# Kernel optimization log

Hardware: AMD Instinct MI355X
Metric: run time of the kernel (lower is better)

## Reference

```python
import jax, jax.numpy as jnp
import numpy as np

B, C, L = 8, 512, 8192
H = 8  # head_count
DK = C // H  # head key channels
DV = C // H  # head value channels


def setup_inputs() -> dict:
    key = jax.random.key(0)
    ks = jax.random.split(key, 10)
    s = 1.0 / np.sqrt(C)
    return {
        "input_": jax.random.normal(ks[0], (B, C, L), jnp.float32),
        "context_": jax.random.normal(ks[1], (B, C, L), jnp.float32),
        "Wk": jax.random.normal(ks[2], (C, C), jnp.float32) * s,
        "bk": jax.random.normal(ks[3], (C,), jnp.float32) * 0.01,
        "Wq": jax.random.normal(ks[4], (C, C), jnp.float32) * s,
        "bq": jax.random.normal(ks[5], (C,), jnp.float32) * 0.01,
        "Wv": jax.random.normal(ks[6], (C, C), jnp.float32) * s,
        "bv": jax.random.normal(ks[7], (C,), jnp.float32) * 0.01,
        "Wr": jax.random.normal(ks[8], (C, C), jnp.float32) * s,
        "br": jax.random.normal(ks[9], (C,), jnp.float32) * 0.01,
    }


def _proj(W, b, x):
    # 1x1 Conv1d == channel matmul: [O,C] x [B,C,L] -> [B,O,L]
    return jnp.einsum('oc,bcl->bol', W, x) + b[None, :, None]


def reference(input_, context_, Wk, bk, Wq, bq, Wv, bv, Wr, br):
    b, _, l = input_.shape
    keys = _proj(Wk, bk, context_).reshape(b, H, DK, l)
    queries = _proj(Wq, bq, input_).reshape(b, H, DK, l)
    values = _proj(Wv, bv, context_).reshape(b, H, DV, l)
    # per-head: softmax(K) over sequence, softmax(Q) over head-key channels
    k = jax.nn.softmax(keys, axis=3)
    q = jax.nn.softmax(queries, axis=2)
    # context = K @ V^T : [b,h,dk,dv]
    ctx = jnp.einsum('bhkl,bhvl->bhkv', k, values)
    # attended = context^T @ Q : [b,h,dv,l]
    att = jnp.einsum('bhkv,bhkl->bhvl', ctx, q).reshape(b, H * DV, l)
    return _proj(Wr, br, att) + input_
```

## Files before the change

kernel.cpp:

```cpp
#include <hip/hip_runtime.h>

#define NB 8
#define NC 512
#define NL 8192
#define NH 8
#define ND 64

typedef float f32x4 __attribute__((ext_vector_type(4)));
typedef __bf16 bf16x8 __attribute__((ext_vector_type(8)));
typedef unsigned int u32x4 __attribute__((ext_vector_type(4)));

__device__ __forceinline__ unsigned short f2bf(float f) {
    unsigned u = __builtin_bit_cast(unsigned, f);
    u += 0x7fffu + ((u >> 16) & 1u);
    return (unsigned short)(u >> 16);
}
__device__ __forceinline__ float bf2f_lo(unsigned w) {
    return __builtin_bit_cast(float, w << 16);
}
__device__ __forceinline__ float bf2f_hi(unsigned w) {
    return __builtin_bit_cast(float, w & 0xffff0000u);
}
__device__ __forceinline__ bf16x8 frag_from_u32x4(u32x4 v) {
    return __builtin_bit_cast(bf16x8, v);
}
__device__ __forceinline__ bf16x8 ld_frag_lds(const unsigned short* p) {
    const unsigned* q = (const unsigned*)p;
    u32x4 v = { q[0], q[1], q[2], q[3] };
    return frag_from_u32x4(v);
}
__device__ __forceinline__ bf16x8 ld_frag_g16(const unsigned short* p) {
    return frag_from_u32x4(*(const u32x4*)p);
}

__device__ __forceinline__ void gload16(const unsigned short* g, unsigned short* l) {
    __builtin_amdgcn_global_load_lds(
        (const __attribute__((address_space(1))) unsigned int*)g,
        (__attribute__((address_space(3))) unsigned int*)l, 16, 0, 0);
}

__global__ __launch_bounds__(256) void cvt_w_kernel(const float* __restrict__ s,
                                                    unsigned short* __restrict__ d, int n) {
    int i = blockIdx.x * 256 + threadIdx.x;
    if (i < n) d[i] = f2bf(s[i]);
}

__global__ __launch_bounds__(256) void zero_kernel(float* __restrict__ p, int n) {
    int i = blockIdx.x * 256 + threadIdx.x;
    if (i < n) p[i] = 0.f;
}

__global__ __launch_bounds__(256) void concat_bias_kernel(const float* __restrict__ a,
                                                          const float* __restrict__ b,
                                                          float* __restrict__ d) {
    int i = blockIdx.x * 256 + threadIdx.x;
    d[i] = (i < NC) ? a[i] : b[i - NC];
}

__device__ __forceinline__ int ltidx(int c, int l) {
    return c * 64 + ((((l) >> 2) ^ ((c >> 2) & 15)) << 2) + (l & 3);
}
__global__ __launch_bounds__(256) void transpose_cvt_kernel(
    const float* __restrict__ X, unsigned short* __restrict__ Y)
{
    const int b = blockIdx.z;
    const int l0 = blockIdx.x * 64, c0 = blockIdx.y * 64;
    const int t = threadIdx.x;
    __shared__ alignas(16) unsigned short lt[64 * 64];
    const float* Xb = X + (size_t)b * NC * NL;
    #pragma unroll
    for (int it = 0; it < 4; ++it) {
        const int c = it * 16 + (t >> 4), l4 = (t & 15) * 4;
        f32x4 v = *(const f32x4*)(Xb + (size_t)(c0 + c) * NL + l0 + l4);
        unsigned lo = f2bf(v.x) | ((unsigned)f2bf(v.y) << 16);
        unsigned hi = f2bf(v.z) | ((unsigned)f2bf(v.w) << 16);
        unsigned* p = (unsigned*)&lt[ltidx(c, l4)];
        p[0] = lo; p[1] = hi;
    }
    __syncthreads();
    unsigned short* Yb = Y + (size_t)b * NL * NC;
    #pragma unroll
    for (int it = 0; it < 2; ++it) {
        const int l = it * 32 + (t >> 3), c8 = (t & 7) * 8;
        u32x4 o;
        #pragma unroll
        for (int d = 0; d < 4; ++d) {
            unsigned lo = lt[ltidx(c8 + 2 * d, l)];
            unsigned hi = lt[ltidx(c8 + 2 * d + 1, l)];
            o[d] = lo | (hi << 16);
        }
        *(u32x4*)(Yb + (size_t)(l0 + l) * NC + c0 + c8) = o;
    }
}

template<int MT, bool RESID, bool PERB, bool QSMT>
__global__ __launch_bounds__(256) void gemm_kernel(
    const unsigned short* __restrict__ Wb,
    const unsigned short* __restrict__ Xt,
    const float* __restrict__ bias,
    const float* __restrict__ resid,
    void* __restrict__ Yv)
{
    const int bx = blockIdx.x;
    const int g  = bx >> 3;
    const int mt = g % MT;
    const int nt = (g / MT) * 8 + (bx & 7);
    const int b  = blockIdx.y;
    const int t  = threadIdx.x;
    const int wave = t >> 6, lane = t & 63;
    const int m0 = mt * 128, n0 = nt * 128;
    const int wm = (wave & 1) * 64, wn = (wave >> 1) * 64;
    const int OC = MT * 128;

    __shared__ alignas(16) unsigned short lA[128 * 32];
    __shared__ alignas(16) unsigned short lX[128 * 32];

    f32x4 acc[4][4] = {};

    const unsigned short* Wp = Wb + (PERB ? (size_t)b * NC * NC : 0);
    const unsigned short* Xb = Xt + (size_t)b * NL * NC;

    const int lr = lane & 15, q = lane >> 4;
    const unsigned aoff = (unsigned)((wm + lr) * 64 + (q ^ (((wm + lr) >> 1) & 3)) * 16);
    const unsigned boff = (unsigned)((wn + lr) * 64 + (q ^ (((wn + lr) >> 1) & 3)) * 16);
    const int pb0 = wave * 128;

    for (int k0 = 0; k0 < NC; k0 += 32) {
        #pragma unroll
        for (int cc = 0; cc < 2; ++cc) {
            const int pb = pb0 + cc * 64;
            const int p  = pb + lane;
            const int r  = p >> 2;
            const int qq = (p & 3) ^ ((r >> 1) & 3);
            gload16(Wp + (size_t)(m0 + r) * NC + k0 + qq * 8, &lA[pb * 8]);
            gload16(Xb + (size_t)(n0 + r) * NC + k0 + qq * 8, &lX[pb * 8]);
        }
        __syncthreads();

        bf16x8 af[4], bfx[4];
        #pragma unroll
        for (int i = 0; i < 4; ++i)
            af[i] = frag_from_u32x4(*(const u32x4*)((const char*)lA + aoff + i * 1024));
        #pragma unroll
        for (int j = 0; j < 4; ++j)
            bfx[j] = frag_from_u32x4(*(const u32x4*)((const char*)lX + boff + j * 1024));
        #pragma unroll
        for (int i = 0; i < 4; ++i)
            #pragma unroll
            for (int j = 0; j < 4; ++j)
                acc[i][j] = __builtin_amdgcn_mfma_f32_16x16x32_bf16(af[i], bfx[j], acc[i][j], 0, 0, 0);
        __syncthreads();
    }

    const int col = lane & 15, row0 = (lane >> 4) * 4;

    if constexpr (QSMT) {
        #pragma unroll
        for (int i = 0; i < 4; ++i)
            #pragma unroll
            for (int r = 0; r < 4; ++r) {
                const float bo = bias[m0 + wm + i * 16 + row0 + r];
                #pragma unroll
                for (int j = 0; j < 4; ++j) acc[i][j][r] += bo;
            }
        float inv[4];
        #pragma unroll
        for (int j = 0; j < 4; ++j) {
            float m = -1e30f;
            #pragma unroll
            for (int i = 0; i < 4; ++i)
                #pragma unroll
                for (int r = 0; r < 4; ++r) m = fmaxf(m, acc[i][j][r]);
            m = fmaxf(m, __shfl_xor(m, 16));
            m = fmaxf(m, __shfl_xor(m, 32));
            float s = 0.f;
            #pragma unroll
            for (int i = 0; i < 4; ++i)
                #pragma unroll
                for (int r = 0; r < 4; ++r) {
                    const float e = __expf(acc[i][j][r] - m);
                    acc[i][j][r] = e;
                    s += e;
                }
            s += __shfl_xor(s, 16);
            s += __shfl_xor(s, 32);
            inv[j] = 1.0f / s;
        }
        unsigned short* Yq = (unsigned short*)Yv;
        #pragma unroll
        for (int j = 0; j < 4; ++j) {
            const size_t rowb = (size_t)b * NL * NC + (size_t)(n0 + wn + j * 16 + col) * NC;
            #pragma unroll
            for (int i = 0; i < 4; ++i) {
                const int o0 = m0 + wm + i * 16 + row0;
                unsigned lo = f2bf(acc[i][j][0] * inv[j]) | ((unsigned)f2bf(acc[i][j][1] * inv[j]) << 16);
                unsigned hi = f2bf(acc[i][j][2] * inv[j]) | ((unsigned)f2bf(acc[i][j][3] * inv[j]) << 16);
                *(unsigned long long*)(Yq + rowb + o0) =
                    (unsigned long long)lo | ((unsigned long long)hi << 32);
            }
        }
    } else {
        #pragma unroll
        for (int i = 0; i < 4; ++i) {
            #pragma unroll
            for (int r = 0; r < 4; ++r) {
                const int o = m0 + wm + i * 16 + row0 + r;
                const float bo = bias[o];
                const size_t rb = (size_t)b * OC * NL + (size_t)o * NL + n0 + wn;
                if constexpr (RESID) {
                    float* Y = (float*)Yv;
                    #pragma unroll
                    for (int j = 0; j < 4; ++j) {
                        const size_t idx = rb + j * 16 + col;
                        Y[idx] = acc[i][j][r] + bo + resid[idx];
                    }
                } else {
                    unsigned short* Y = (unsigned short*)Yv;
                    #pragma unroll
                    for (int j = 0; j < 4; ++j)
                        Y[rb + j * 16 + col] = f2bf(acc[i][j][r] + bo);
                }
            }
        }
    }
}

__global__ __launch_bounds__(256) void softmax_rows(unsigned short* __restrict__ KV) {
    const int row = blockIdx.x;
    const int t = threadIdx.x;
    const int wave = t >> 6, lane = t & 63;
    unsigned short* p = KV + ((size_t)(row >> 9) * 2 * NC + (row & 511)) * NL;

    float v[32];
    float mx = -1e30f;
    #pragma unroll
    for (int i = 0; i < 4; ++i) {
        u32x4 raw = *(const u32x4*)(p + (size_t)(i * 256 + t) * 8);
        #pragma unroll
        for (int d = 0; d < 4; ++d) {
            unsigned w = raw[d];
            v[i * 8 + d * 2]     = bf2f_lo(w);
            v[i * 8 + d * 2 + 1] = bf2f_hi(w);
        }
        #pragma unroll
        for (int j = 0; j < 8; ++j) mx = fmaxf(mx, v[i * 8 + j]);
    }
    #pragma unroll
    for (int off = 32; off > 0; off >>= 1) mx = fmaxf(mx, __shfl_down(mx, off));
    __shared__ float red[16];
    if (lane == 0) red[wave] = mx;
    __syncthreads();
    mx = fmaxf(fmaxf(red[0], red[1]), fmaxf(red[2], red[3]));

    float s = 0.f;
    #pragma unroll
    for (int i = 0; i < 32; ++i) { v[i] = __expf(v[i] - mx); s += v[i]; }
    #pragma unroll
    for (int off = 32; off > 0; off >>= 1) s += __shfl_down(s, off);
    if (lane == 0) red[8 + wave] = s;
    __syncthreads();
    s = red[8] + red[9] + red[10] + red[11];
    const float inv = 1.0f / s;

    #pragma unroll
    for (int i = 0; i < 4; ++i) {
        u32x4 outw;
        #pragma unroll
        for (int d = 0; d < 4; ++d) {
            unsigned lo = f2bf(v[i * 8 + d * 2] * inv);
            unsigned hi = f2bf(v[i * 8 + d * 2 + 1] * inv);
            outw[d] = lo | (hi << 16);
        }
        *(u32x4*)(p + (size_t)(i * 256 + t) * 8) = outw;
    }
}

__global__ __launch_bounds__(256) void ctx_kernel(
    const unsigned short* __restrict__ KV,
    float* __restrict__ ctx)
{
    const int bh = blockIdx.x;
    const int sp = blockIdx.y;
    const int t = threadIdx.x;
    const int wave = t >> 6, lane = t & 63;
    const int b = bh >> 3, h = bh & 7;
    const size_t base_k = ((size_t)b * 2 * NC + h * ND) * NL;
    const size_t base_v = base_k + (size_t)NC * NL;
    const int i = wave * 16 + (lane & 15);
    const int koff = (lane >> 4) * 8;
    const unsigned short* Ka = KV + base_k + (size_t)i * NL + koff;

    f32x4 acc[4] = {};
    const int l0 = sp * (NL / 16);
    for (int l = l0; l < l0 + (NL / 16); l += 32) {
        bf16x8 a = ld_frag_g16(Ka + l);
        #pragma unroll
        for (int j = 0; j < 4; ++j) {
            bf16x8 bv = ld_frag_g16(KV + base_v + (size_t)(j * 16 + (lane & 15)) * NL + l + koff);
            acc[j] = __builtin_amdgcn_mfma_f32_16x16x32_bf16(a, bv, acc[j], 0, 0, 0);
        }
    }
    const int col = lane & 15, row0 = (lane >> 4) * 4;
    #pragma unroll
    for (int j = 0; j < 4; ++j)
        #pragma unroll
        for (int r = 0; r < 4; ++r)
            atomicAdd(&ctx[(size_t)bh * (ND * ND) + (size_t)(wave * 16 + row0 + r) * ND + j * 16 + col],
                      acc[j][r]);
}

__global__ __launch_bounds__(512) void fold_kernel(
    const unsigned short* __restrict__ Wrb,
    const float* __restrict__ ctxb,
    unsigned short* __restrict__ Mb)
{
    const int bh = blockIdx.x;
    const int b = bh >> 3, h = bh & 7;
    const int t = threadIdx.x;
    const int wave = t >> 6, lane = t & 63;

    __shared__ unsigned short lc[64 * 66];
    const float* cs = ctxb + (size_t)bh * (ND * ND);
    #pragma unroll
    for (int it = 0; it < 8; ++it) {
        int i = it * 512 + t;
        lc[(i >> 6) * 66 + (i & 63)] = f2bf(cs[i]);
    }
    __syncthreads();

    const int koff = (lane >> 4) * 8;
    f32x4 acc[4][4] = {};
    #pragma unroll
    for (int kk = 0; kk < 64; kk += 32) {
        bf16x8 af[4], bfx[4];
        #pragma unroll
        for (int i = 0; i < 4; ++i)
            af[i] = ld_frag_g16(Wrb + (size_t)(wave * 64 + i * 16 + (lane & 15)) * NC
                                + h * ND + kk + koff);
        #pragma unroll
        for (int j = 0; j < 4; ++j)
            bfx[j] = ld_frag_lds(&lc[(j * 16 + (lane & 15)) * 66 + kk + koff]);
        #pragma unroll
        for (int i = 0; i < 4; ++i)
            #pragma unroll
            for (int j = 0; j < 4; ++j)
                acc[i][j] = __builtin_amdgcn_mfma_f32_16x16x32_bf16(af[i], bfx[j], acc[i][j], 0, 0, 0);
    }

    const int col = lane & 15, row0 = (lane >> 4) * 4;
    #pragma unroll
    for (int i = 0; i < 4; ++i)
        #pragma unroll
        for (int r = 0; r < 4; ++r) {
            const int o = wave * 64 + i * 16 + row0 + r;
            #pragma unroll
            for (int j = 0; j < 4; ++j)
                Mb[(size_t)b * NC * NC + (size_t)o * NC + h * ND + j * 16 + col]
                    = f2bf(acc[i][j][r]);
        }
}

extern "C" void kernel_launch(void* const* d_in, const int* in_sizes, int n_in,
                              void* d_out, int out_size, void* d_ws, size_t ws_size,
                              hipStream_t stream) {
    (void)in_sizes; (void)n_in; (void)out_size; (void)ws_size;
    const float* input_   = (const float*)d_in[0];
    const float* context_ = (const float*)d_in[1];
    const float* Wk = (const float*)d_in[2];
    const float* bk = (const float*)d_in[3];
    const float* Wq = (const float*)d_in[4];
    const float* bq = (const float*)d_in[5];
    const float* Wv = (const float*)d_in[6];
    const float* bv = (const float*)d_in[7];
    const float* Wr = (const float*)d_in[8];
    const float* br = (const float*)d_in[9];
    float* out = (float*)d_out;

    char* ws = (char*)d_ws;
    unsigned short* Wkvb = (unsigned short*)ws;
    unsigned short* Wqb  = Wkvb + 2 * NC * NC;
    unsigned short* Wrb  = Wqb + NC * NC;
    float* bkv  = (float*)(Wrb + NC * NC);
    float* ctxb = bkv + 2 * NC;
    unsigned short* KVp = (unsigned short*)(ctxb + NB * NH * ND * ND);
    unsigned short* R2  = KVp + (size_t)NB * 2 * NC * NL;
    unsigned short* Mb  = KVp;
    unsigned short* Xt_in = (unsigned short*)d_out;

    const int wN = NC * NC;
    cvt_w_kernel<<<wN / 256, 256, 0, stream>>>(Wk, Wkvb, wN);
    cvt_w_kernel<<<wN / 256, 256, 0, stream>>>(Wv, Wkvb + wN, wN);
    cvt_w_kernel<<<wN / 256, 256, 0, stream>>>(Wq, Wqb, wN);
    cvt_w_kernel<<<wN / 256, 256, 0, stream>>>(Wr, Wrb, wN);
    concat_bias_kernel<<<4, 256, 0, stream>>>(bk, bv, bkv);
    zero_kernel<<<(NB * NH * ND * ND) / 256, 256, 0, stream>>>(ctxb, NB * NH * ND * ND);

    transpose_cvt_kernel<<<dim3(NL / 64, NC / 64, NB), 256, 0, stream>>>(context_, R2);

    gemm_kernel<8, false, false, false><<<dim3(64 * 8, NB), 256, 0, stream>>>(
        Wkvb, R2, bkv, nullptr, KVp);

    transpose_cvt_kernel<<<dim3(NL / 64, NC / 64, NB), 256, 0, stream>>>(input_, Xt_in);

    gemm_kernel<4, false, false, true><<<dim3(64 * 4, NB), 256, 0, stream>>>(
        Wqb, Xt_in, bq, nullptr, R2);

    softmax_rows<<<NB * NC, 256, 0, stream>>>(KVp);
    ctx_kernel<<<dim3(NB * NH, 16), 256, 0, stream>>>(KVp, ctxb);
    fold_kernel<<<NB * NH, 512, 0, stream>>>(Wrb, ctxb, Mb);

    gemm_kernel<4, true, true, false><<<dim3(64 * 4, NB), 256, 0, stream>>>(
        Mb, R2, br, input_, out);
}
```

Before: 654.6 us.

## Fuse key softmax into KV GEMM epilogue, merge prep and transpose launches, widen K tile

```diff
diff --git a/kernel.cpp b/kernel.cpp
--- a/kernel.cpp
+++ b/kernel.cpp
@@ -15,12 +15,6 @@
     u += 0x7fffu + ((u >> 16) & 1u);
     return (unsigned short)(u >> 16);
 }
-__device__ __forceinline__ float bf2f_lo(unsigned w) {
-    return __builtin_bit_cast(float, w << 16);
-}
-__device__ __forceinline__ float bf2f_hi(unsigned w) {
-    return __builtin_bit_cast(float, w & 0xffff0000u);
-}
 __device__ __forceinline__ bf16x8 frag_from_u32x4(u32x4 v) {
     return __builtin_bit_cast(bf16x8, v);
 }
@@ -39,31 +33,38 @@
         (__attribute__((address_space(3))) unsigned int*)l, 16, 0, 0);
 }
 
-__global__ __launch_bounds__(256) void cvt_w_kernel(const float* __restrict__ s,
-                                                    unsigned short* __restrict__ d, int n) {
+__global__ __launch_bounds__(256) void prep_kernel(
+    const float* __restrict__ Wk, const float* __restrict__ Wv,
+    const float* __restrict__ Wq, const float* __restrict__ Wr,
+    const float* __restrict__ bk, const float* __restrict__ bv,
+    unsigned short* __restrict__ Wb,
+    float* __restrict__ bkv,
+    float* __restrict__ zf)
+{
+    const int WN = NC * NC;
     int i = blockIdx.x * 256 + threadIdx.x;
-    if (i < n) d[i] = f2bf(s[i]);
-}
-
-__global__ __launch_bounds__(256) void zero_kernel(float* __restrict__ p, int n) {
-    int i = blockIdx.x * 256 + threadIdx.x;
-    if (i < n) p[i] = 0.f;
-}
-
-__global__ __launch_bounds__(256) void concat_bias_kernel(const float* __restrict__ a,
-                                                          const float* __restrict__ b,
-                                                          float* __restrict__ d) {
-    int i = blockIdx.x * 256 + threadIdx.x;
-    d[i] = (i < NC) ? a[i] : b[i - NC];
+    if (i < 4 * WN) {
+        const float* src = (i < WN) ? Wk : (i < 2 * WN) ? Wv : (i < 3 * WN) ? Wq : Wr;
+        Wb[i] = f2bf(src[i & (WN - 1)]);
+    } else if (i < 4 * WN + 2 * NC) {
+        int j = i - 4 * WN;
+        bkv[j] = (j < NC) ? bk[j] : bv[j - NC];
+    } else {
+        zf[i - (4 * WN + 2 * NC)] = 0.f;
+    }
 }
 
 __device__ __forceinline__ int ltidx(int c, int l) {
     return c * 64 + ((((l) >> 2) ^ ((c >> 2) & 15)) << 2) + (l & 3);
 }
 __global__ __launch_bounds__(256) void transpose_cvt_kernel(
-    const float* __restrict__ X, unsigned short* __restrict__ Y)
+    const float* __restrict__ X0, const float* __restrict__ X1,
+    unsigned short* __restrict__ Y0, unsigned short* __restrict__ Y1)
 {
-    const int b = blockIdx.z;
+    const int bz = blockIdx.z;
+    const float* X = (bz < NB) ? X0 : X1;
+    unsigned short* Y = (bz < NB) ? Y0 : Y1;
+    const int b = bz & (NB - 1);
     const int l0 = blockIdx.x * 64, c0 = blockIdx.y * 64;
     const int t = threadIdx.x;
     __shared__ alignas(16) unsigned short lt[64 * 64];
@@ -93,13 +94,14 @@
     }
 }
 
-template<int MT, bool RESID, bool PERB, bool QSMT>
+template<int MT, bool RESID, bool PERB, bool QSMT, bool EXPK>
 __global__ __launch_bounds__(256) void gemm_kernel(
     const unsigned short* __restrict__ Wb,
     const unsigned short* __restrict__ Xt,
     const float* __restrict__ bias,
     const float* __restrict__ resid,
-    void* __restrict__ Yv)
+    void* __restrict__ Yv,
+    float* __restrict__ rowsum)
 {
     const int bx = blockIdx.x;
     const int g  = bx >> 3;
@@ -112,8 +114,8 @@
     const int wm = (wave & 1) * 64, wn = (wave >> 1) * 64;
     const int OC = MT * 128;
 
-    __shared__ alignas(16) unsigned short lA[128 * 32];
-    __shared__ alignas(16) unsigned short lX[128 * 32];
+    __shared__ alignas(16) unsigned short lA[128 * 64];
+    __shared__ alignas(16) unsigned short lX[128 * 64];
 
     f32x4 acc[4][4] = {};
 
@@ -121,34 +123,38 @@
     const unsigned short* Xb = Xt + (size_t)b * NL * NC;
 
     const int lr = lane & 15, q = lane >> 4;
-    const unsigned aoff = (unsigned)((wm + lr) * 64 + (q ^ (((wm + lr) >> 1) & 3)) * 16);
-    const unsigned boff = (unsigned)((wn + lr) * 64 + (q ^ (((wn + lr) >> 1) & 3)) * 16);
-    const int pb0 = wave * 128;
-
-    for (int k0 = 0; k0 < NC; k0 += 32) {
-        #pragma unroll
-        for (int cc = 0; cc < 2; ++cc) {
-            const int pb = pb0 + cc * 64;
+    const unsigned abase = (unsigned)((wm + lr) * 128);
+    const unsigned bbase = (unsigned)((wn + lr) * 128);
+    const unsigned sw = (unsigned)(lr & 7);
+
+    for (int k0 = 0; k0 < NC; k0 += 64) {
+        #pragma unroll
+        for (int cc = 0; cc < 4; ++cc) {
+            const int pb = wave * 256 + cc * 64;
             const int p  = pb + lane;
-            const int r  = p >> 2;
-            const int qq = (p & 3) ^ ((r >> 1) & 3);
+            const int r  = p >> 3;
+            const int qq = (p & 7) ^ (r & 7);
             gload16(Wp + (size_t)(m0 + r) * NC + k0 + qq * 8, &lA[pb * 8]);
             gload16(Xb + (size_t)(n0 + r) * NC + k0 + qq * 8, &lX[pb * 8]);
         }
         __syncthreads();
 
-        bf16x8 af[4], bfx[4];
-        #pragma unroll
-        for (int i = 0; i < 4; ++i)
-            af[i] = frag_from_u32x4(*(const u32x4*)((const char*)lA + aoff + i * 1024));
-        #pragma unroll
-        for (int j = 0; j < 4; ++j)
-            bfx[j] = frag_from_u32x4(*(const u32x4*)((const char*)lX + boff + j * 1024));
-        #pragma unroll
-        for (int i = 0; i < 4; ++i)
+        #pragma unroll
+        for (int kk = 0; kk < 2; ++kk) {
+            const unsigned cq = (((unsigned)(kk * 4 + q)) ^ sw) * 16;
+            bf16x8 af[4], bfx[4];
+            #pragma unroll
+            for (int i = 0; i < 4; ++i)
+                af[i] = frag_from_u32x4(*(const u32x4*)((const char*)lA + abase + i * 2048 + cq));
             #pragma unroll
             for (int j = 0; j < 4; ++j)
-                acc[i][j] = __builtin_amdgcn_mfma_f32_16x16x32_bf16(af[i], bfx[j], acc[i][j], 0, 0, 0);
+                bfx[j] = frag_from_u32x4(*(const u32x4*)((const char*)lX + bbase + j * 2048 + cq));
+            #pragma unroll
+            for (int i = 0; i < 4; ++i)
+                #pragma unroll
+                for (int j = 0; j < 4; ++j)
+                    acc[i][j] = __builtin_amdgcn_mfma_f32_16x16x32_bf16(af[i], bfx[j], acc[i][j], 0, 0, 0);
+        }
         __syncthreads();
     }
 
@@ -198,6 +204,40 @@
                 *(unsigned long long*)(Yq + rowb + o0) =
                     (unsigned long long)lo | ((unsigned long long)hi << 32);
             }
+        }
+    } else if constexpr (EXPK) {
+        unsigned short* Y = (unsigned short*)Yv;
+        if (m0 < NC) {
+            #pragma unroll
+            for (int i = 0; i < 4; ++i)
+                #pragma unroll
+                for (int r = 0; r < 4; ++r) {
+                    const int o = m0 + wm + i * 16 + row0 + r;
+                    const float bo = bias[o];
+                    const size_t rb = (size_t)b * OC * NL + (size_t)o * NL + n0 + wn;
+                    float ps = 0.f;
+                    #pragma unroll
+                    for (int j = 0; j < 4; ++j) {
+                        const float e = __expf(acc[i][j][r] + bo);
+                        ps += e;
+                        Y[rb + j * 16 + col] = f2bf(e);
+                    }
+                    #pragma unroll
+                    for (int off = 1; off < 16; off <<= 1) ps += __shfl_xor(ps, off);
+                    if (col == 0) atomicAdd(&rowsum[(size_t)b * NC + o], ps);
+                }
+        } else {
+            #pragma unroll
+            for (int i = 0; i < 4; ++i)
+                #pragma unroll
+                for (int r = 0; r < 4; ++r) {
+                    const int o = m0 + wm + i * 16 + row0 + r;
+                    const float bo = bias[o];
+                    const size_t rb = (size_t)b * OC * NL + (size_t)o * NL + n0 + wn;
+                    #pragma unroll
+                    for (int j = 0; j < 4; ++j)
+                        Y[rb + j * 16 + col] = f2bf(acc[i][j][r] + bo);
+                }
         }
     } else {
         #pragma unroll
@@ -225,56 +265,6 @@
     }
 }
 
-__global__ __launch_bounds__(256) void softmax_rows(unsigned short* __restrict__ KV) {
-    const int row = blockIdx.x;
-    const int t = threadIdx.x;
-    const int wave = t >> 6, lane = t & 63;
-    unsigned short* p = KV + ((size_t)(row >> 9) * 2 * NC + (row & 511)) * NL;
-
-    float v[32];
-    float mx = -1e30f;
-    #pragma unroll
-    for (int i = 0; i < 4; ++i) {
-        u32x4 raw = *(const u32x4*)(p + (size_t)(i * 256 + t) * 8);
-        #pragma unroll
-        for (int d = 0; d < 4; ++d) {
-            unsigned w = raw[d];
-            v[i * 8 + d * 2]     = bf2f_lo(w);
-            v[i * 8 + d * 2 + 1] = bf2f_hi(w);
-        }
-        #pragma unroll
-        for (int j = 0; j < 8; ++j) mx = fmaxf(mx, v[i * 8 + j]);
-    }
-    #pragma unroll
-    for (int off = 32; off > 0; off >>= 1) mx = fmaxf(mx, __shfl_down(mx, off));
-    __shared__ float red[16];
-    if (lane == 0) red[wave] = mx;
-    __syncthreads();
-    mx = fmaxf(fmaxf(red[0], red[1]), fmaxf(red[2], red[3]));
-
-    float s = 0.f;
-    #pragma unroll
-    for (int i = 0; i < 32; ++i) { v[i] = __expf(v[i] - mx); s += v[i]; }
-    #pragma unroll
-    for (int off = 32; off > 0; off >>= 1) s += __shfl_down(s, off);
-    if (lane == 0) red[8 + wave] = s;
-    __syncthreads();
-    s = red[8] + red[9] + red[10] + red[11];
-    const float inv = 1.0f / s;
-
-    #pragma unroll
-    for (int i = 0; i < 4; ++i) {
-        u32x4 outw;
-        #pragma unroll
-        for (int d = 0; d < 4; ++d) {
-            unsigned lo = f2bf(v[i * 8 + d * 2] * inv);
-            unsigned hi = f2bf(v[i * 8 + d * 2 + 1] * inv);
-            outw[d] = lo | (hi << 16);
-        }
-        *(u32x4*)(p + (size_t)(i * 256 + t) * 8) = outw;
-    }
-}
-
 __global__ __launch_bounds__(256) void ctx_kernel(
     const unsigned short* __restrict__ KV,
     float* __restrict__ ctx)
@@ -312,6 +302,7 @@
 __global__ __launch_bounds__(512) void fold_kernel(
     const unsigned short* __restrict__ Wrb,
     const float* __restrict__ ctxb,
+    const float* __restrict__ rowsum,
     unsigned short* __restrict__ Mb)
 {
     const int bh = blockIdx.x;
@@ -321,10 +312,11 @@
 
     __shared__ unsigned short lc[64 * 66];
     const float* cs = ctxb + (size_t)bh * (ND * ND);
+    const float* rs = rowsum + (size_t)b * NC + h * ND;
     #pragma unroll
     for (int it = 0; it < 8; ++it) {
         int i = it * 512 + t;
-        lc[(i >> 6) * 66 + (i & 63)] = f2bf(cs[i]);
+        lc[(i >> 6) * 66 + (i & 63)] = f2bf(cs[i] / rs[i >> 6]);
     }
     __syncthreads();
 
@@ -382,33 +374,29 @@
     unsigned short* Wrb  = Wqb + NC * NC;
     float* bkv  = (float*)(Wrb + NC * NC);
     float* ctxb = bkv + 2 * NC;
-    unsigned short* KVp = (unsigned short*)(ctxb + NB * NH * ND * ND);
+    float* rowsum = ctxb + NB * NH * ND * ND;
+    unsigned short* KVp = (unsigned short*)(rowsum + NB * NC);
     unsigned short* R2  = KVp + (size_t)NB * 2 * NC * NL;
     unsigned short* Mb  = KVp;
     unsigned short* Xt_in = (unsigned short*)d_out;
 
-    const int wN = NC * NC;
-    cvt_w_kernel<<<wN / 256, 256, 0, stream>>>(Wk, Wkvb, wN);
-    cvt_w_kernel<<<wN / 256, 256, 0, stream>>>(Wv, Wkvb + wN, wN);
-    cvt_w_kernel<<<wN / 256, 256, 0, stream>>>(Wq, Wqb, wN);
-    cvt_w_kernel<<<wN / 256, 256, 0, stream>>>(Wr, Wrb, wN);
-    concat_bias_kernel<<<4, 256, 0, stream>>>(bk, bv, bkv);
-    zero_kernel<<<(NB * NH * ND * ND) / 256, 256, 0, stream>>>(ctxb, NB * NH * ND * ND);
-
-    transpose_cvt_kernel<<<dim3(NL / 64, NC / 64, NB), 256, 0, stream>>>(context_, R2);
-
-    gemm_kernel<8, false, false, false><<<dim3(64 * 8, NB), 256, 0, stream>>>(
-        Wkvb, R2, bkv, nullptr, KVp);
-
-    transpose_cvt_kernel<<<dim3(NL / 64, NC / 64, NB), 256, 0, stream>>>(input_, Xt_in);
-
-    gemm_kernel<4, false, false, true><<<dim3(64 * 4, NB), 256, 0, stream>>>(
-        Wqb, Xt_in, bq, nullptr, R2);
-
-    softmax_rows<<<NB * NC, 256, 0, stream>>>(KVp);
+    const int WN = NC * NC;
+    const int prep_elems = 4 * WN + 2 * NC + (NB * NH * ND * ND + NB * NC);
+    prep_kernel<<<(prep_elems + 255) / 256, 256, 0, stream>>>(
+        Wk, Wv, Wq, Wr, bk, bv, Wkvb, bkv, ctxb);
+
+    transpose_cvt_kernel<<<dim3(NL / 64, NC / 64, 2 * NB), 256, 0, stream>>>(
+        context_, input_, R2, Xt_in);
+
+    gemm_kernel<8, false, false, false, true><<<dim3(64 * 8, NB), 256, 0, stream>>>(
+        Wkvb, R2, bkv, nullptr, KVp, rowsum);
+
+    gemm_kernel<4, false, false, true, false><<<dim3(64 * 4, NB), 256, 0, stream>>>(
+        Wqb, Xt_in, bq, nullptr, R2, nullptr);
+
     ctx_kernel<<<dim3(NB * NH, 16), 256, 0, stream>>>(KVp, ctxb);
-    fold_kernel<<<NB * NH, 512, 0, stream>>>(Wrb, ctxb, Mb);
-
-    gemm_kernel<4, true, true, false><<<dim3(64 * 4, NB), 256, 0, stream>>>(
-        Mb, R2, br, input_, out);
-}
+    fold_kernel<<<NB * NH, 512, 0, stream>>>(Wrb, ctxb, rowsum, Mb);
+
+    gemm_kernel<4, true, true, false, false><<<dim3(64 * 4, NB), 256, 0, stream>>>(
+        Mb, R2, br, input_, out, nullptr);
+}
```

Measured after the change: 707.7 us. +8.1%, slower.
